# Kernel optimization log

Hardware: AMD Instinct MI355X
Metric: run time of the kernel (lower is better)

The kernel has to match this reference:

```python
import jax, jax.numpy as jnp
import numpy as np

HEADS = 4
HID = 610
KER = 50  # cov2KerSize
NEG_SLOPE = 0.2


def gat_layer(x, src, dst, w, b, att_src, att_dst, n_nodes):
    # x: [N, Fin], w: [HEADS*HID, Fin], att_*: [1, HEADS, HID], b: [HID]
    h = (x @ w.T).reshape(n_nodes, HEADS, HID)               # [N,H,D]
    a_src = (h * att_src).sum(-1)                            # [N,H]
    a_dst = (h * att_dst).sum(-1)                            # [N,H]
    alpha = jax.nn.leaky_relu(a_src[src] + a_dst[dst], NEG_SLOPE)  # [E,H]
    # softmax over edges grouped by destination node
    m = jax.ops.segment_max(alpha, dst, num_segments=n_nodes)
    e = jnp.exp(alpha - m[dst])
    denom = jax.ops.segment_sum(e, dst, num_segments=n_nodes)
    a = e / (denom[dst] + 1e-16)                             # [E,H]
    msg = h[src] * a[:, :, None]                             # [E,H,D]
    out = jax.ops.segment_sum(msg, dst, num_segments=n_nodes)  # [N,H,D]
    return out.mean(axis=1) + b                              # [N,D] (concat=False)


def setup_inputs() -> dict:
    key = jax.random.key(0)
    ks = jax.random.split(key, 16)
    N, E, FIN, NOUT = 20000, 100000, 128, 86
    x = jax.random.normal(ks[0], (N, FIN), dtype=jnp.float32)
    edge_index = jax.random.randint(ks[1], (2, E), 0, N, dtype=jnp.int64)
    def kaiming(k, shape, fan_in):
        return jax.random.normal(k, shape, dtype=jnp.float32) * np.float32(np.sqrt(2.0 / fan_in))
    w0 = kaiming(ks[2], (HEADS * HID, FIN), FIN)
    b0 = jnp.zeros((HID,), jnp.float32)
    att_src0 = kaiming(ks[3], (1, HEADS, HID), HID)
    att_dst0 = kaiming(ks[4], (1, HEADS, HID), HID)
    w2 = kaiming(ks[5], (HEADS * HID, HID), HID)
    b2 = jnp.zeros((HID,), jnp.float32)
    att_src1 = kaiming(ks[6], (1, HEADS, HID), HID)
    att_dst1 = kaiming(ks[7], (1, HEADS, HID), HID)
    w4 = kaiming(ks[8], (1, 1, 2, KER), 2 * KER)
    b4 = jnp.zeros((1,), jnp.float32)
    w6 = kaiming(ks[9], (1, 1, KER), KER)
    b6 = jnp.zeros((1,), jnp.float32)
    w8 = kaiming(ks[10], (NOUT, 512), 512)
    b8 = jnp.zeros((NOUT,), jnp.float32)
    return dict(x=x, edge_index=edge_index, w0=w0, b0=b0, att_src0=att_src0,
                att_dst0=att_dst0, w2=w2, b2=b2, att_src1=att_src1,
                att_dst1=att_dst1, w4=w4, b4=b4, w6=w6, b6=b6, w8=w8, b8=b8)


def reference(x, edge_index, w0, b0, att_src0, att_dst0, w2, b2, att_src1,
              att_dst1, w4, b4, w6, b6, w8, b8):
    N = x.shape[0]
    src, dst = edge_index[0], edge_index[1]
    x1 = jax.nn.relu(gat_layer(x, src, dst, w0, b0, att_src0, att_dst0, N))
    x2 = jax.nn.relu(gat_layer(x1, src, dst, w2, b2, att_src1, att_dst1, N))
    # edge features: cat(src_feat, dst_feat) viewed as [E,1,2,HID]
    ef = jnp.stack([x2[src], x2[dst]], axis=1)[:, None, :, :]  # [E,1,2,HID]
    y = jax.lax.conv_general_dilated(ef, w4, (1, 1), 'VALID',
                                     dimension_numbers=('NCHW', 'OIHW', 'NCHW'))
    y = jax.nn.relu(y + b4[None, :, None, None])               # [E,1,1,561]
    y = y.reshape(-1, HID - KER + 1, 1).transpose(0, 2, 1)     # [E,1,561]
    y = jax.lax.conv_general_dilated(y, w6, (1,), 'VALID',
                                     dimension_numbers=('NCH', 'OIH', 'NCH'))
    y = jax.nn.relu(y + b6[None, :, None])                     # [E,1,512]
    # adaptive_avg_pool1d to 512 is identity since length is already 512
    y = y.reshape(-1, 512)
    return y @ w8.T + b8                                       # [E, num_outputs]
```

## Files before the change

### kernel.cpp

```cpp
#include <hip/hip_runtime.h>
#include <math.h>

#define HEADS 4
#define HID 610
#define HIDP 640
#define FIN 128
#define KER 50
#define NOUT 86
#define NEG_SLOPE 0.2f

#define Y1S 616
#define ZSS 520

typedef short bf8_t __attribute__((ext_vector_type(8)));
typedef float f4_t __attribute__((ext_vector_type(4)));

__device__ __forceinline__ ushort f2bf(float f) {
    unsigned u = __float_as_uint(f);
    unsigned r = (u + 0x7FFFu + ((u >> 16) & 1u)) >> 16;
    return (ushort)r;
}
__device__ __forceinline__ ushort f2bf_t(float f) {
    return (ushort)(__float_as_uint(f) >> 16);
}
__device__ __forceinline__ float bf2f(ushort b) { return __uint_as_float(((unsigned)b) << 16); }

__device__ __forceinline__ void gload16(const void* g, void* l) {
    __builtin_amdgcn_global_load_lds((const __attribute__((address_space(1))) void*)g,
                                     (__attribute__((address_space(3))) void*)l, 16, 0, 0);
}

__global__ void fill_val(float* __restrict__ p, float v, long n) {
    long i = (long)blockIdx.x * blockDim.x + threadIdx.x;
    if (i < n) p[i] = v;
}

__global__ void copy_int(const int* __restrict__ a, int* __restrict__ b, int n) {
    int i = blockIdx.x * blockDim.x + threadIdx.x;
    if (i < n) b[i] = a[i];
}

__global__ void hist_k(const int* __restrict__ ei, int* __restrict__ hist, int E) {
    int e = blockIdx.x * blockDim.x + threadIdx.x;
    if (e < E) atomicAdd(&hist[ei[E + e]], 1);
}

__global__ __launch_bounds__(1024) void scan_k(const int* __restrict__ hist,
                                               int* __restrict__ base, int Nn) {
    __shared__ int tmp[1024];
    __shared__ int carry;
    if (threadIdx.x == 0) carry = 0;
    __syncthreads();
    for (int c0 = 0; c0 < Nn; c0 += 1024) {
        int i = c0 + threadIdx.x;
        int v = (i < Nn) ? hist[i] : 0;
        tmp[threadIdx.x] = v;
        __syncthreads();
        for (int off = 1; off < 1024; off <<= 1) {
            int t = (threadIdx.x >= off) ? tmp[threadIdx.x - off] : 0;
            __syncthreads();
            tmp[threadIdx.x] += t;
            __syncthreads();
        }
        if (i < Nn) base[i] = carry + tmp[threadIdx.x] - v;
        __syncthreads();
        if (threadIdx.x == 1023) carry += tmp[1023];
        __syncthreads();
    }
    if (threadIdx.x == 0) base[Nn] = carry;
}

__global__ void scatter_k(const int* __restrict__ ei, int* __restrict__ cursor,
                          int* __restrict__ esrc, int* __restrict__ edst,
                          int* __restrict__ eorg, int E) {
    int e = blockIdx.x * blockDim.x + threadIdx.x;
    if (e >= E) return;
    int d = ei[E + e];
    int pos = atomicAdd(&cursor[d], 1);
    esrc[pos] = ei[e];
    edst[pos] = d;
    eorg[pos] = e;
}

__global__ void split_pad(const float* __restrict__ in, ushort* __restrict__ hi,
                          ushort* __restrict__ lo, int R, int K, int Kp) {
    long i = (long)blockIdx.x * blockDim.x + threadIdx.x;
    if (i >= (long)R * Kp) return;
    int r = (int)(i / Kp), c = (int)(i % Kp);
    float v = (c < K) ? in[(long)r * K + c] : 0.f;
    ushort h = f2bf(v);
    hi[i] = h;
    lo[i] = f2bf(v - bf2f(h));
}

__global__ void build_toeplitz(const float* __restrict__ w4, const float* __restrict__ w6,
                               ushort* __restrict__ T) {
    int i = blockIdx.x * blockDim.x + threadIdx.x;
    if (i >= 18 * 512) return;
    int e = i & 7;
    int lane = (i >> 3) & 63;
    int f = i >> 9;
    int n = lane & 15;
    int k = ((lane >> 4) << 3) + e;
    float wv;
    int hilo;
    if (f < 12) {
        int c = f % 3, hc = f / 3;
        int ch = hc & 1;
        hilo = hc >> 1;
        int d = c * 32 + k - n;
        wv = (d >= 0 && d < KER) ? w4[ch * KER + d] : 0.f;
    } else {
        int r2 = f - 12;
        int c = r2 % 3;
        hilo = r2 / 3;
        int d = c * 32 + k - n;
        wv = (d >= 0 && d < KER) ? w6[d] : 0.f;
    }
    ushort h = f2bf(wv);
    T[i] = hilo ? f2bf(wv - bf2f(h)) : h;
}

template <int AMODE, bool BIAS>
__global__ __launch_bounds__(256) void gemm_mfma(const float* __restrict__ A,
                                                 const ushort* __restrict__ Aghi,
                                                 const ushort* __restrict__ Aglo,
                                                 const ushort* __restrict__ Bghi,
                                                 const ushort* __restrict__ Bglo,
                                                 const float* __restrict__ bias,
                                                 float* __restrict__ C,
                                                 int M, int N, int Kp) {
    __shared__ __align__(16) ushort Ah[128 * 32];
    __shared__ __align__(16) ushort Al[128 * 32];
    __shared__ __align__(16) ushort Bh[128 * 32];
    __shared__ __align__(16) ushort Bl[128 * 32];
    int tid = threadIdx.x;
    int wave = tid >> 6, lane = tid & 63;
    int quad = lane >> 4, l16 = lane & 15;
    int wm = wave & 1, wn = wave >> 1;
    int row0 = blockIdx.y * 128, col0 = blockIdx.x * 128;

    f4_t acc[4][4];
#pragma unroll
    for (int i = 0; i < 4; i++)
#pragma unroll
        for (int j = 0; j < 4; j++) acc[i][j] = (f4_t){0.f, 0.f, 0.f, 0.f};

    int sw = (quad ^ ((l16 >> 1) & 3)) << 3;
    auto compute_tile = [&]() {
        bf8_t ah[4], al[4], bh[4], bl[4];
#pragma unroll
        for (int t = 0; t < 4; t++) {
            int ar = wm * 64 + t * 16 + l16;
            ah[t] = *(const bf8_t*)&Ah[ar * 32 + sw];
            al[t] = *(const bf8_t*)&Al[ar * 32 + sw];
            int br = wn * 64 + t * 16 + l16;
            bh[t] = *(const bf8_t*)&Bh[br * 32 + sw];
            bl[t] = *(const bf8_t*)&Bl[br * 32 + sw];
        }
#pragma unroll
        for (int i = 0; i < 4; i++)
#pragma unroll
            for (int j = 0; j < 4; j++) {
                acc[i][j] = __builtin_amdgcn_mfma_f32_16x16x32_bf16(ah[i], bh[j], acc[i][j], 0, 0, 0);
                acc[i][j] = __builtin_amdgcn_mfma_f32_16x16x32_bf16(al[i], bh[j], acc[i][j], 0, 0, 0);
                acc[i][j] = __builtin_amdgcn_mfma_f32_16x16x32_bf16(ah[i], bl[j], acc[i][j], 0, 0, 0);
            }
    };

    if constexpr (AMODE == 0) {
        float4 pa0[4];
        uint4 pbh[2], pbl[2];
        auto loadA = [&](int k0) {
#pragma unroll
            for (int q = 0; q < 4; q++) {
                int p = tid + q * 256;
                int r = p >> 3, c4 = (p & 7) << 2;
                int gr = row0 + r;
                pa0[q] = (gr < M) ? *(const float4*)(A + (size_t)gr * Kp + k0 + c4)
                                  : make_float4(0.f, 0.f, 0.f, 0.f);
            }
        };
        auto loadB = [&](int k0) {
#pragma unroll
            for (int q = 0; q < 2; q++) {
                int p = tid + q * 256;
                int r = p >> 2, c = p & 3;
                int gr = col0 + r;
                if (gr < N) {
                    pbh[q] = *(const uint4*)(Bghi + (size_t)gr * Kp + k0 + c * 8);
                    pbl[q] = *(const uint4*)(Bglo + (size_t)gr * Kp + k0 + c * 8);
                } else {
                    pbh[q] = make_uint4(0, 0, 0, 0);
                    pbl[q] = make_uint4(0, 0, 0, 0);
                }
            }
        };
        auto writeLDS = [&]() {
#pragma unroll
            for (int q = 0; q < 4; q++) {
                int p = tid + q * 256;
                int r = p >> 3, m = p & 7;
                int pos = r * 32 + ((((m >> 1)) ^ ((r >> 1) & 3)) << 3) + ((m & 1) << 2);
                float4 v = pa0[q];
                ushort4 hv, lv;
                hv.x = f2bf(v.x); lv.x = f2bf(v.x - bf2f(hv.x));
                hv.y = f2bf(v.y); lv.y = f2bf(v.y - bf2f(hv.y));
                hv.z = f2bf(v.z); lv.z = f2bf(v.z - bf2f(hv.z));
                hv.w = f2bf(v.w); lv.w = f2bf(v.w - bf2f(hv.w));
                *(ushort4*)&Ah[pos] = hv;
                *(ushort4*)&Al[pos] = lv;
            }
#pragma unroll
            for (int q = 0; q < 2; q++) {
                int p = tid + q * 256;
                int r = p >> 2, c = p & 3;
                int pos = r * 32 + ((c ^ ((r >> 1) & 3)) << 3);
                *(uint4*)&Bh[pos] = pbh[q];
                *(uint4*)&Bl[pos] = pbl[q];
            }
        };
        loadA(0);
        loadB(0);
        for (int k0 = 0; k0 < Kp; k0 += 32) {
            __syncthreads();
            writeLDS();
            __syncthreads();
            if (k0 + 32 < Kp) {
                loadA(k0 + 32);
                loadB(k0 + 32);
            }
            compute_tile();
        }
    } else {
        const int r_ = lane >> 2, cs = lane & 3;
        for (int k0 = 0; k0 < Kp; k0 += 32) {
            __syncthreads();
#pragma unroll
            for (int q = 0; q < 2; q++) {
                const int r0 = wave * 32 + q * 16;
                const int r = r0 + r_;
                const int ca = cs ^ ((r >> 1) & 3);
                const size_t goA = (size_t)(row0 + r) * Kp + k0 + ca * 8;
                const size_t goB = (size_t)(col0 + r) * Kp + k0 + ca * 8;
                gload16(Aghi + goA, &Ah[r0 * 32]);
                gload16(Aglo + goA, &Al[r0 * 32]);
                gload16(Bghi + goB, &Bh[r0 * 32]);
                gload16(Bglo + goB, &Bl[r0 * 32]);
            }
            __syncthreads();
            compute_tile();
        }
    }

#pragma unroll
    for (int i = 0; i < 4; i++) {
#pragma unroll
        for (int r = 0; r < 4; r++) {
            int grow = row0 + wm * 64 + i * 16 + quad * 4 + r;
            if (grow >= M) continue;
#pragma unroll
            for (int j = 0; j < 4; j++) {
                int gcol = col0 + wn * 64 + j * 16 + l16;
                if (gcol >= N) continue;
                float v = acc[i][j][r];
                if (BIAS) v += bias[gcol];
                C[(size_t)grow * N + gcol] = v;
            }
        }
    }
}

__global__ __launch_bounds__(256) void attn_dots(const float* __restrict__ h,
                                                 const float* __restrict__ att_s,
                                                 const float* __restrict__ att_d,
                                                 float* __restrict__ a_src,
                                                 float* __restrict__ a_dst, int Nn) {
    int n = blockIdx.x;
    int head = threadIdx.x >> 6;
    int lane = threadIdx.x & 63;
    const float2* hr = (const float2*)(h + (long)n * (HEADS * HID) + head * HID);
    const float2* as = (const float2*)(att_s + head * HID);
    const float2* ad = (const float2*)(att_d + head * HID);
    float ss = 0.f, sd = 0.f;
    for (int d = lane; d < HID / 2; d += 64) {
        float2 hv = hr[d], av = as[d], dv = ad[d];
        ss += hv.x * av.x + hv.y * av.y;
        sd += hv.x * dv.x + hv.y * dv.y;
    }
    for (int off = 32; off > 0; off >>= 1) {
        ss += __shfl_down(ss, off);
        sd += __shfl_down(sd, off);
    }
    if (lane == 0) {
        a_src[n * HEADS + head] = ss;
        a_dst[n * HEADS + head] = sd;
    }
}

template <int OUTMODE>
__global__ __launch_bounds__(256) void node_aggregate(
    const float* __restrict__ h, const float* __restrict__ asrc,
    const float* __restrict__ adst, const int* __restrict__ base,
    const int* __restrict__ esrc, const float* __restrict__ bias,
    float* __restrict__ xout, ushort* __restrict__ xhi, ushort* __restrict__ xlo,
    int Nn) {
    int wave = threadIdx.x >> 6, lane = threadIdx.x & 63;
    int n = blockIdx.x * 4 + wave;
    if (n >= Nn) return;
    int b0 = base[n], deg = base[n + 1] - b0;
    float ad[HEADS];
#pragma unroll
    for (int hh = 0; hh < HEADS; hh++) ad[hh] = adst[n * HEADS + hh];
    float m[HEADS] = {-INFINITY, -INFINITY, -INFINITY, -INFINITY};
    for (int eb = 0; eb < deg; eb += 64) {
        int i = eb + lane;
        if (i < deg) {
            int s = esrc[b0 + i];
#pragma unroll
            for (int hh = 0; hh < HEADS; hh++) {
                float v = asrc[s * HEADS + hh] + ad[hh];
                v = v >= 0.f ? v : NEG_SLOPE * v;
                m[hh] = fmaxf(m[hh], v);
            }
        }
    }
#pragma unroll
    for (int off = 32; off > 0; off >>= 1)
#pragma unroll
        for (int hh = 0; hh < HEADS; hh++) m[hh] = fmaxf(m[hh], __shfl_xor(m[hh], off));
    float sden[HEADS] = {0.f, 0.f, 0.f, 0.f};
    for (int eb = 0; eb < deg; eb += 64) {
        int i = eb + lane;
        if (i < deg) {
            int s = esrc[b0 + i];
#pragma unroll
            for (int hh = 0; hh < HEADS; hh++) {
                float v = asrc[s * HEADS + hh] + ad[hh];
                v = v >= 0.f ? v : NEG_SLOPE * v;
                sden[hh] += expf(v - m[hh]);
            }
        }
    }
#pragma unroll
    for (int off = 32; off > 0; off >>= 1)
#pragma unroll
        for (int hh = 0; hh < HEADS; hh++) sden[hh] += __shfl_xor(sden[hh], off);
    float inv[HEADS];
#pragma unroll
    for (int hh = 0; hh < HEADS; hh++) inv[hh] = 0.25f / (sden[hh] + 1e-16f);
    float2 acc0[5] = {}, acc1[5] = {}, acc2[5] = {}, acc3[5] = {};
    for (int eb = 0; eb < deg; eb += 64) {
        int i = eb + lane;
        int sreg = 0;
        float coef[HEADS] = {0.f, 0.f, 0.f, 0.f};
        if (i < deg) {
            sreg = esrc[b0 + i];
#pragma unroll
            for (int hh = 0; hh < HEADS; hh++) {
                float v = asrc[sreg * HEADS + hh] + ad[hh];
                v = v >= 0.f ? v : NEG_SLOPE * v;
                coef[hh] = expf(v - m[hh]) * inv[hh];
            }
        }
        int cnt = deg - eb < 64 ? deg - eb : 64;
        for (int j = 0; j < cnt; j++) {
            int s = __shfl(sreg, j);
            float c0 = __shfl(coef[0], j), c1 = __shfl(coef[1], j);
            float c2 = __shfl(coef[2], j), c3 = __shfl(coef[3], j);
            const float2* hr = (const float2*)(h + (size_t)s * (HEADS * HID));
#pragma unroll
            for (int t = 0; t < 5; t++) {
                int d = lane + t * 64;
                if (d < HID / 2) {
                    float2 v0 = hr[d];
                    float2 v1 = hr[HID / 2 + d];
                    float2 v2 = hr[HID + d];
                    float2 v3 = hr[3 * (HID / 2) + d];
                    acc0[t].x = fmaf(c0, v0.x, acc0[t].x);
                    acc0[t].y = fmaf(c0, v0.y, acc0[t].y);
                    acc1[t].x = fmaf(c1, v1.x, acc1[t].x);
                    acc1[t].y = fmaf(c1, v1.y, acc1[t].y);
                    acc2[t].x = fmaf(c2, v2.x, acc2[t].x);
                    acc2[t].y = fmaf(c2, v2.y, acc2[t].y);
                    acc3[t].x = fmaf(c3, v3.x, acc3[t].x);
                    acc3[t].y = fmaf(c3, v3.y, acc3[t].y);
                }
            }
        }
    }
#pragma unroll
    for (int t = 0; t < 5; t++) {
        int d = lane + t * 64;
        if (d < HID / 2) {
            float2 bb = *(const float2*)&bias[2 * d];
            float vx = acc0[t].x + acc1[t].x + acc2[t].x + acc3[t].x + bb.x;
            float vy = acc0[t].y + acc1[t].y + acc2[t].y + acc3[t].y + bb.y;
            vx = vx > 0.f ? vx : 0.f;
            vy = vy > 0.f ? vy : 0.f;
            if (OUTMODE == 0) {
                *(float2*)&xout[(size_t)n * HIDP + 2 * d] = make_float2(vx, vy);
            } else {
                ushort hx = f2bf(vx), hy = f2bf(vy);
                ushort2 hv; hv.x = hx; hv.y = hy;
                ushort2 lv; lv.x = f2bf(vx - bf2f(hx)); lv.y = f2bf(vy - bf2f(hy));
                *(ushort2*)&xhi[(size_t)n * HIDP + 2 * d] = hv;
                *(ushort2*)&xlo[(size_t)n * HIDP + 2 * d] = lv;
            }
        }
    }
    for (int d = HID + lane; d < HIDP; d += 64) {
        if (OUTMODE == 0) {
            xout[(size_t)n * HIDP + d] = 0.f;
        } else {
            xhi[(size_t)n * HIDP + d] = 0;
            xlo[(size_t)n * HIDP + d] = 0;
        }
    }
}

__global__ __launch_bounds__(256, 3) void edge_fused(
    const ushort* __restrict__ x2hi, const ushort* __restrict__ x2lo,
    const int* __restrict__ esrc, const int* __restrict__ edst,
    const int* __restrict__ eorg, const ushort* __restrict__ T,
    const float* __restrict__ b4, const float* __restrict__ b6,
    const ushort* __restrict__ w8hi, const ushort* __restrict__ w8lo,
    const float* __restrict__ b8, float* __restrict__ out, int E) {
    __shared__ __align__(16) ushort y1h[16 * Y1S];
    __shared__ __align__(16) ushort y1l[16 * Y1S];
    const int tid = threadIdx.x;
    const int wave = tid >> 6, lane = tid & 63;
    const int quad = lane >> 4, l16 = lane & 15;
    const int e0 = blockIdx.x * 16;
    const int p = wave & 1;
    const int half = wave >> 1;
    const int p16 = p * 16;

    int i = e0 + l16;
    if (i >= E) i = E - 1;
    const int s = esrc[i], d = edst[i];
    const ushort* psh = x2hi + (size_t)s * HIDP + quad * 8;
    const ushort* psl = x2lo + (size_t)s * HIDP + quad * 8;
    const ushort* pth = x2hi + (size_t)d * HIDP + quad * 8;
    const ushort* ptl = x2lo + (size_t)d * HIDP + quad * 8;

    bf8_t Wsh[6], Wsl[6], Wth[6], Wtl[6];
#define LDCH(slot, m)                                     \
    {                                                     \
        const int o_ = p16 + 32 * (m);                    \
        Wsh[slot] = *(const bf8_t*)(psh + o_);            \
        Wth[slot] = *(const bf8_t*)(pth + o_);            \
        if ((m) <= 18) {                                  \
            Wsl[slot] = *(const bf8_t*)(psl + o_);        \
            Wtl[slot] = *(const bf8_t*)(ptl + o_);        \
        }                                                 \
    }
    const int t0 = half * 9;
#pragma unroll
    for (int m = 0; m < 5; m++) LDCH(m, t0 + m);

    for (int idx = tid; idx < 16 * (Y1S - 576); idx += 256) {
        int r = idx / (Y1S - 576);
        int j = 576 + (idx - r * (Y1S - 576));
        y1h[r * Y1S + j] = 0;
        y1l[r * Y1S + j] = 0;
    }

    bf8_t B1h[2][3], B1l[2][2];
#pragma unroll
    for (int ch = 0; ch < 2; ch++) {
#pragma unroll
        for (int c = 0; c < 3; c++)
            B1h[ch][c] = *(const bf8_t*)&T[(ch * 3 + c) * 512 + lane * 8];
#pragma unroll
        for (int c = 0; c < 2; c++)
            B1l[ch][c] = *(const bf8_t*)&T[((2 + ch) * 3 + c) * 512 + lane * 8];
    }
    const float bb4 = b4[0], bb6 = b6[0];

#pragma unroll
    for (int tt = 0; tt < 9; tt++) {
        if (tt <= 5) LDCH((tt + 5) % 6, t0 + tt + 5);
        const int c0 = tt % 6, c1 = (tt + 1) % 6, c2 = (tt + 2) % 6;
        f4_t acc = {bb4, bb4, bb4, bb4};
        acc = __builtin_amdgcn_mfma_f32_16x16x32_bf16(Wsh[c0], B1h[0][0], acc, 0, 0, 0);
        acc = __builtin_amdgcn_mfma_f32_16x16x32_bf16(Wsl[c0], B1h[0][0], acc, 0, 0, 0);
        acc = __builtin_amdgcn_mfma_f32_16x16x32_bf16(Wsh[c0], B1l[0][0], acc, 0, 0, 0);
        acc = __builtin_amdgcn_mfma_f32_16x16x32_bf16(Wth[c0], B1h[1][0], acc, 0, 0, 0);
        acc = __builtin_amdgcn_mfma_f32_16x16x32_bf16(Wtl[c0], B1h[1][0], acc, 0, 0, 0);
        acc = __builtin_amdgcn_mfma_f32_16x16x32_bf16(Wth[c0], B1l[1][0], acc, 0, 0, 0);
        acc = __builtin_amdgcn_mfma_f32_16x16x32_bf16(Wsh[c1], B1h[0][1], acc, 0, 0, 0);
        acc = __builtin_amdgcn_mfma_f32_16x16x32_bf16(Wsl[c1], B1h[0][1], acc, 0, 0, 0);
        acc = __builtin_amdgcn_mfma_f32_16x16x32_bf16(Wsh[c1], B1l[0][1], acc, 0, 0, 0);
        acc = __builtin_amdgcn_mfma_f32_16x16x32_bf16(Wth[c1], B1h[1][1], acc, 0, 0, 0);
        acc = __builtin_amdgcn_mfma_f32_16x16x32_bf16(Wtl[c1], B1h[1][1], acc, 0, 0, 0);
        acc = __builtin_amdgcn_mfma_f32_16x16x32_bf16(Wth[c1], B1l[1][1], acc, 0, 0, 0);
        acc = __builtin_amdgcn_mfma_f32_16x16x32_bf16(Wsh[c2], B1h[0][2], acc, 0, 0, 0);
        acc = __builtin_amdgcn_mfma_f32_16x16x32_bf16(Wth[c2], B1h[1][2], acc, 0, 0, 0);
        const int j0 = p16 + 32 * (t0 + tt);
#pragma unroll
        for (int r = 0; r < 4; r++) {
            int e_ = quad * 4 + r;
            int pos = e_ * Y1S + j0 + l16;
            float v = acc[r];
            v = v > 0.f ? v : 0.f;
            ushort hh = f2bf_t(v);
            y1h[pos] = hh;
            y1l[pos] = f2bf(v - bf2f(hh));
        }
    }
    __syncthreads();

    bf8_t B2h[3], B2l[2];
#pragma unroll
    for (int c = 0; c < 3; c++) B2h[c] = *(const bf8_t*)&T[(12 + c) * 512 + lane * 8];
#pragma unroll
    for (int c = 0; c < 2; c++) B2l[c] = *(const bf8_t*)&T[(15 + c) * 512 + lane * 8];
    const int arow1 = l16 * Y1S + quad * 8;
    bf8_t Yh[4], Yl[4];
#define LDY(slot, m)                                          \
    {                                                         \
        const int o_ = arow1 + p16 + 32 * (m);                \
        Yh[slot] = *(const bf8_t*)&y1h[o_];                   \
        if ((m) <= 16) Yl[slot] = *(const bf8_t*)&y1l[o_];    \
    }
    const int t0b = half * 8;
#pragma unroll
    for (int m = 0; m < 3; m++) LDY(m, t0b + m);
    f4_t zac[8];
#pragma unroll
    for (int tt = 0; tt < 8; tt++) {
        if (tt <= 6) LDY((tt + 3) & 3, t0b + tt + 3);
        const int c0 = tt & 3, c1 = (tt + 1) & 3, c2 = (tt + 2) & 3;
        f4_t acc = {bb6, bb6, bb6, bb6};
        acc = __builtin_amdgcn_mfma_f32_16x16x32_bf16(Yh[c0], B2h[0], acc, 0, 0, 0);
        acc = __builtin_amdgcn_mfma_f32_16x16x32_bf16(Yl[c0], B2h[0], acc, 0, 0, 0);
        acc = __builtin_amdgcn_mfma_f32_16x16x32_bf16(Yh[c0], B2l[0], acc, 0, 0, 0);
        acc = __builtin_amdgcn_mfma_f32_16x16x32_bf16(Yh[c1], B2h[1], acc, 0, 0, 0);
        acc = __builtin_amdgcn_mfma_f32_16x16x32_bf16(Yl[c1], B2h[1], acc, 0, 0, 0);
        acc = __builtin_amdgcn_mfma_f32_16x16x32_bf16(Yh[c1], B2l[1], acc, 0, 0, 0);
        acc = __builtin_amdgcn_mfma_f32_16x16x32_bf16(Yh[c2], B2h[2], acc, 0, 0, 0);
#pragma unroll
        for (int r = 0; r < 4; r++) {
            float v = acc[r];
            zac[tt][r] = v > 0.f ? v : 0.f;
        }
    }
    __syncthreads();

#pragma unroll
    for (int tt = 0; tt < 8; tt++) {
        const int j02 = p16 + 32 * (t0b + tt);
#pragma unroll
        for (int r = 0; r < 4; r++) {
            int e_ = quad * 4 + r;
            int pos = e_ * ZSS + j02 + l16;
            float v = zac[tt][r];
            ushort hh = f2bf_t(v);
            y1h[pos] = hh;
            y1l[pos] = f2bf(v - bf2f(hh));
        }
    }
    __syncthreads();

#pragma unroll
    for (int it = 0; it < 2; it++) {
        const int nt = wave + it * 4;
        if (nt < 6) {
            const int col = nt * 16 + l16;
            const int wrow = col < NOUT ? col : 0;
            const float bias = col < NOUT ? b8[col] : 0.f;
            f4_t acc = {bias, bias, bias, bias};
            const int arow = l16 * ZSS + quad * 8;
            const ushort* wph = w8hi + (size_t)wrow * 512 + quad * 8;
            const ushort* wpl = w8lo + (size_t)wrow * 512 + quad * 8;
#pragma unroll
            for (int c = 0; c < 16; c++) {
                bf8_t zh = *(const bf8_t*)&y1h[arow + c * 32];
                bf8_t zl = *(const bf8_t*)&y1l[arow + c * 32];
                bf8_t wh = *(const bf8_t*)(wph + c * 32);
                bf8_t wl = *(const bf8_t*)(wpl + c * 32);
                acc = __builtin_amdgcn_mfma_f32_16x16x32_bf16(zh, wh, acc, 0, 0, 0);
                acc = __builtin_amdgcn_mfma_f32_16x16x32_bf16(zl, wh, acc, 0, 0, 0);
                acc = __builtin_amdgcn_mfma_f32_16x16x32_bf16(zh, wl, acc, 0, 0, 0);
            }
            if (col < NOUT) {
#pragma unroll
                for (int r = 0; r < 4; r++) {
                    int er = e0 + quad * 4 + r;
                    if (er < E) out[(size_t)eorg[er] * NOUT + col] = acc[r];
                }
            }
        }
    }
#undef LDCH
#undef LDY
}

extern "C" void kernel_launch(void* const* d_in, const int* in_sizes, int n_in,
                              void* d_out, int out_size, void* d_ws, size_t ws_size,
                              hipStream_t stream) {
    const float* x = (const float*)d_in[0];
    const int* ei = (const int*)d_in[1];
    const float* w0 = (const float*)d_in[2];
    const float* b0 = (const float*)d_in[3];
    const float* att_s0 = (const float*)d_in[4];
    const float* att_d0 = (const float*)d_in[5];
    const float* w2 = (const float*)d_in[6];
    const float* b2 = (const float*)d_in[7];
    const float* att_s1 = (const float*)d_in[8];
    const float* att_d1 = (const float*)d_in[9];
    const float* w4 = (const float*)d_in[10];
    const float* b4 = (const float*)d_in[11];
    const float* w6 = (const float*)d_in[12];
    const float* b6 = (const float*)d_in[13];
    const float* w8 = (const float*)d_in[14];
    const float* b8 = (const float*)d_in[15];
    float* out = (float*)d_out;

    const int Nn = in_sizes[0] / FIN;
    const int E = in_sizes[1] / 2;
    const int HD = HEADS * HID;

    float* ws = (float*)d_ws;
    size_t o = 0;
    float* buf1 = ws + o; o += (size_t)Nn * HIDP;
    ushort* x1hi = (ushort*)buf1;
    ushort* x1lo = x1hi + (size_t)Nn * HIDP;
    ushort* w8hi = (ushort*)(ws + o);
    ushort* w8lo = w8hi + (size_t)NOUT * 512; o += (size_t)NOUT * 512;
    int* base = (int*)(ws + o); o += (size_t)Nn + 4;
    int* cursor = (int*)(ws + o); o += (size_t)Nn;
    int* esrc = (int*)(ws + o); o += (size_t)E;
    int* edst = (int*)(ws + o); o += (size_t)E;
    int* eorg = (int*)(ws + o); o += (size_t)E;
    float* asrc = ws + o; o += (size_t)Nn * HEADS;
    float* adst = ws + o; o += (size_t)Nn * HEADS;
    ushort* w0hi = (ushort*)(ws + o);
    ushort* w0lo = w0hi + (size_t)HD * FIN; o += (size_t)HD * FIN;
    ushort* w2hi = (ushort*)(ws + o);
    ushort* w2lo = w2hi + (size_t)HD * HIDP; o += (size_t)HD * HIDP;
    float* h = ws + o;

    int edgeGrid = (E + 255) / 256;
    int nodeWaveGrid = (Nn + 3) / 4;
    int fusedGrid = (E + 15) / 16;
    dim3 gGemmL((HD + 127) / 128, (Nn + 127) / 128);

    split_pad<<<((HD * FIN) + 255) / 256, 256, 0, stream>>>(w0, w0hi, w0lo, HD, FIN, FIN);
    split_pad<<<((HD * HIDP) + 255) / 256, 256, 0, stream>>>(w2, w2hi, w2lo, HD, HID, HIDP);
    split_pad<<<((NOUT * 512) + 255) / 256, 256, 0, stream>>>(w8, w8hi, w8lo, NOUT, 512, 512);
    fill_val<<<(Nn + 255) / 256, 256, 0, stream>>>((float*)cursor, 0.f, Nn);
    hist_k<<<edgeGrid, 256, 0, stream>>>(ei, cursor, E);
    scan_k<<<1, 1024, 0, stream>>>(cursor, base, Nn);
    copy_int<<<(Nn + 255) / 256, 256, 0, stream>>>(base, cursor, Nn);
    scatter_k<<<edgeGrid, 256, 0, stream>>>(ei, cursor, esrc, edst, eorg, E);

    gemm_mfma<0, false><<<gGemmL, 256, 0, stream>>>(x, nullptr, nullptr, w0hi, w0lo, nullptr,
                                                    h, Nn, HD, FIN);
    build_toeplitz<<<(18 * 512 + 255) / 256, 256, 0, stream>>>(w4, w6, w0hi);
    attn_dots<<<Nn, 256, 0, stream>>>(h, att_s0, att_d0, asrc, adst, Nn);
    node_aggregate<1><<<nodeWaveGrid, 256, 0, stream>>>(h, asrc, adst, base, esrc, b0,
                                                        nullptr, x1hi, x1lo, Nn);

    gemm_mfma<1, false><<<gGemmL, 256, 0, stream>>>(nullptr, x1hi, x1lo, w2hi, w2lo, nullptr,
                                                    h, Nn, HD, HIDP);
    attn_dots<<<Nn, 256, 0, stream>>>(h, att_s1, att_d1, asrc, adst, Nn);
    node_aggregate<1><<<nodeWaveGrid, 256, 0, stream>>>(h, asrc, adst, base, esrc, b2,
                                                        nullptr, x1hi, x1lo, Nn);

    edge_fused<<<fusedGrid, 256, 0, stream>>>(x1hi, x1lo, esrc, edst, eorg, w0hi, b4, b6,
                                              w8hi, w8lo, b8, out, E);
}
```

Measured before the change: 1.057 ms.

## Fold attention dot products into GEMM via precomputed W^T·att columns

Precomputes eight extra weight rows (att_src/att_dst projected through W per head) and appends them as extra output columns of the projection GEMM, so a_src/a_dst come out of the GEMM epilogue directly. This removes the two attn_dots kernels that reread the full h tensor. HD=2440 already needs 20 column tiles and HD+8 still fits in them, so the grid does not grow; only the last tile does more work. The extra rows are stored in the cursor buffer, which is reused after the scatter, and the bf16 hi/lo split of the folded weights slightly changes the rounding of the attention logits.

Result: slower. 1.087 ms (+2.8%).

```diff
diff --git a/kernel.cpp b/kernel.cpp
--- a/kernel.cpp
+++ b/kernel.cpp
@@ -91,6 +91,24 @@
     ushort h = f2bf(v);
     hi[i] = h;
     lo[i] = f2bf(v - bf2f(h));
+}
+
+__global__ void build_watt(const float* __restrict__ w, const float* __restrict__ att_s,
+                           const float* __restrict__ att_d, ushort* __restrict__ exthi,
+                           ushort* __restrict__ extlo, int K, int Kp) {
+    int i = blockIdx.x * blockDim.x + threadIdx.x;
+    if (i >= 8 * Kp) return;
+    int e = i / Kp, k = i - e * Kp;
+    int hh = e & 3;
+    const float* att = (e < 4) ? att_s : att_d;
+    float acc = 0.f;
+    if (k < K) {
+        for (int d = 0; d < HID; d++)
+            acc += att[hh * HID + d] * w[(size_t)(hh * HID + d) * K + k];
+    }
+    ushort h_ = f2bf(acc);
+    exthi[i] = h_;
+    extlo[i] = f2bf(acc - bf2f(h_));
 }
 
 __global__ void build_toeplitz(const float* __restrict__ w4, const float* __restrict__ w6,
@@ -127,9 +145,13 @@
                                                  const ushort* __restrict__ Aglo,
                                                  const ushort* __restrict__ Bghi,
                                                  const ushort* __restrict__ Bglo,
+                                                 const ushort* __restrict__ Bexthi,
+                                                 const ushort* __restrict__ Bextlo,
                                                  const float* __restrict__ bias,
                                                  float* __restrict__ C,
-                                                 int M, int N, int Kp) {
+                                                 float* __restrict__ aout_s,
+                                                 float* __restrict__ aout_d,
+                                                 int M, int Nb, int N0, int Kp) {
     __shared__ __align__(16) ushort Ah[128 * 32];
     __shared__ __align__(16) ushort Al[128 * 32];
     __shared__ __align__(16) ushort Bh[128 * 32];
@@ -187,9 +209,12 @@
                 int p = tid + q * 256;
                 int r = p >> 2, c = p & 3;
                 int gr = col0 + r;
-                if (gr < N) {
+                if (gr < N0) {
                     pbh[q] = *(const uint4*)(Bghi + (size_t)gr * Kp + k0 + c * 8);
                     pbl[q] = *(const uint4*)(Bglo + (size_t)gr * Kp + k0 + c * 8);
+                } else if (gr < Nb) {
+                    pbh[q] = *(const uint4*)(Bexthi + (size_t)(gr - N0) * Kp + k0 + c * 8);
+                    pbl[q] = *(const uint4*)(Bextlo + (size_t)(gr - N0) * Kp + k0 + c * 8);
                 } else {
                     pbh[q] = make_uint4(0, 0, 0, 0);
                     pbl[q] = make_uint4(0, 0, 0, 0);
@@ -242,11 +267,22 @@
                 const int r = r0 + r_;
                 const int ca = cs ^ ((r >> 1) & 3);
                 const size_t goA = (size_t)(row0 + r) * Kp + k0 + ca * 8;
-                const size_t goB = (size_t)(col0 + r) * Kp + k0 + ca * 8;
+                const int gr = col0 + r;
+                const ushort* bh_src;
+                const ushort* bl_src;
+                if (gr < N0) {
+                    bh_src = Bghi + (size_t)gr * Kp;
+                    bl_src = Bglo + (size_t)gr * Kp;
+                } else {
+                    int er = gr - N0;
+                    er = er < 7 ? er : 7;
+                    bh_src = Bexthi + (size_t)er * Kp;
+                    bl_src = Bextlo + (size_t)er * Kp;
+                }
                 gload16(Aghi + goA, &Ah[r0 * 32]);
                 gload16(Aglo + goA, &Al[r0 * 32]);
-                gload16(Bghi + goB, &Bh[r0 * 32]);
-                gload16(Bglo + goB, &Bl[r0 * 32]);
+                gload16(bh_src + k0 + ca * 8, &Bh[r0 * 32]);
+                gload16(bl_src + k0 + ca * 8, &Bl[r0 * 32]);
             }
             __syncthreads();
             compute_tile();
@@ -262,39 +298,18 @@
 #pragma unroll
             for (int j = 0; j < 4; j++) {
                 int gcol = col0 + wn * 64 + j * 16 + l16;
-                if (gcol >= N) continue;
+                if (gcol >= Nb) continue;
                 float v = acc[i][j][r];
-                if (BIAS) v += bias[gcol];
-                C[(size_t)grow * N + gcol] = v;
-            }
-        }
-    }
-}
-
-__global__ __launch_bounds__(256) void attn_dots(const float* __restrict__ h,
-                                                 const float* __restrict__ att_s,
-                                                 const float* __restrict__ att_d,
-                                                 float* __restrict__ a_src,
-                                                 float* __restrict__ a_dst, int Nn) {
-    int n = blockIdx.x;
-    int head = threadIdx.x >> 6;
-    int lane = threadIdx.x & 63;
-    const float2* hr = (const float2*)(h + (long)n * (HEADS * HID) + head * HID);
-    const float2* as = (const float2*)(att_s + head * HID);
-    const float2* ad = (const float2*)(att_d + head * HID);
-    float ss = 0.f, sd = 0.f;
-    for (int d = lane; d < HID / 2; d += 64) {
-        float2 hv = hr[d], av = as[d], dv = ad[d];
-        ss += hv.x * av.x + hv.y * av.y;
-        sd += hv.x * dv.x + hv.y * dv.y;
-    }
-    for (int off = 32; off > 0; off >>= 1) {
-        ss += __shfl_down(ss, off);
-        sd += __shfl_down(sd, off);
-    }
-    if (lane == 0) {
-        a_src[n * HEADS + head] = ss;
-        a_dst[n * HEADS + head] = sd;
+                if (gcol < N0) {
+                    if (BIAS) v += bias[gcol];
+                    C[(size_t)grow * N0 + gcol] = v;
+                } else {
+                    int ec = gcol - N0;
+                    if (ec < 4) aout_s[grow * HEADS + ec] = v;
+                    else aout_d[grow * HEADS + (ec - 4)] = v;
+                }
+            }
+        }
     }
 }
 
@@ -642,10 +657,16 @@
     ushort* w2lo = w2hi + (size_t)HD * HIDP; o += (size_t)HD * HIDP;
     float* h = ws + o;
 
+    ushort* wa1hi = (ushort*)cursor;
+    ushort* wa1lo = wa1hi + 8 * FIN;
+    ushort* wa2hi = wa1lo + 8 * FIN;
+    ushort* wa2lo = wa2hi + 8 * HIDP;
+
     int edgeGrid = (E + 255) / 256;
     int nodeWaveGrid = (Nn + 3) / 4;
     int fusedGrid = (E + 15) / 16;
-    dim3 gGemmL((HD + 127) / 128, (Nn + 127) / 128);
+    dim3 gGemmL((HD + 8 + 127) / 128, (Nn + 127) / 128);
+    dim3 gGemmF((NOUT + 127) / 128, (E + 127) / 128);
 
     split_pad<<<((HD * FIN) + 255) / 256, 256, 0, stream>>>(w0, w0hi, w0lo, HD, FIN, FIN);
     split_pad<<<((HD * HIDP) + 255) / 256, 256, 0, stream>>>(w2, w2hi, w2lo, HD, HID, HIDP);
@@ -655,17 +676,21 @@
     scan_k<<<1, 1024, 0, stream>>>(cursor, base, Nn);
     copy_int<<<(Nn + 255) / 256, 256, 0, stream>>>(base, cursor, Nn);
     scatter_k<<<edgeGrid, 256, 0, stream>>>(ei, cursor, esrc, edst, eorg, E);
-
-    gemm_mfma<0, false><<<gGemmL, 256, 0, stream>>>(x, nullptr, nullptr, w0hi, w0lo, nullptr,
-                                                    h, Nn, HD, FIN);
+    build_watt<<<(8 * FIN + 255) / 256, 256, 0, stream>>>(w0, att_s0, att_d0, wa1hi, wa1lo,
+                                                          FIN, FIN);
+    build_watt<<<(8 * HIDP + 255) / 256, 256, 0, stream>>>(w2, att_s1, att_d1, wa2hi, wa2lo,
+                                                           HID, HIDP);
+
+    gemm_mfma<0, false><<<gGemmL, 256, 0, stream>>>(x, nullptr, nullptr, w0hi, w0lo,
+                                                    wa1hi, wa1lo, nullptr, h, asrc, adst,
+                                                    Nn, HD + 8, HD, FIN);
     build_toeplitz<<<(18 * 512 + 255) / 256, 256, 0, stream>>>(w4, w6, w0hi);
-    attn_dots<<<Nn, 256, 0, stream>>>(h, att_s0, att_d0, asrc, adst, Nn);
     node_aggregate<1><<<nodeWaveGrid, 256, 0, stream>>>(h, asrc, adst, base, esrc, b0,
                                                         nullptr, x1hi, x1lo, Nn);
 
-    gemm_mfma<1, false><<<gGemmL, 256, 0, stream>>>(nullptr, x1hi, x1lo, w2hi, w2lo, nullptr,
-                                                    h, Nn, HD, HIDP);
-    attn_dots<<<Nn, 256, 0, stream>>>(h, att_s1, att_d1, asrc, adst, Nn);
+    gemm_mfma<1, false><<<gGemmL, 256, 0, stream>>>(nullptr, x1hi, x1lo, w2hi, w2lo,
+                                                    wa2hi, wa2lo, nullptr, h, asrc, adst,
+                                                    Nn, HD + 8, HD, HIDP);
     node_aggregate<1><<<nodeWaveGrid, 256, 0, stream>>>(h, asrc, adst, base, esrc, b2,
                                                         nullptr, x1hi, x1lo, Nn);
 
```
